# Optimization experiments

Measured on AMD Instinct MI355X. Metric: run time of the kernel, lower is better.

Reference implementation:

```python
import jax, jax.numpy as jnp
import numpy as np

P = 0.5  # dropout fraction (init kwarg p)


def setup_inputs() -> dict:
    key = jax.random.key(0)
    # positive weights (e.g. post-softmax attention), shape [B, M, N]
    w = jax.random.uniform(key, (8192, 1, 4096), dtype=jnp.float32, minval=1e-4, maxval=1.0)
    return {"w": w}


def reference(w) -> jnp.ndarray:
    # Drop the bottom int(N*P) entries along dim 2 (per row), then renormalize
    # the surviving entries with a softmax over them; dropped entries stay 0.
    B, M, N = w.shape
    k = int(N * P)  # number of smallest entries zeroed per row
    if k == 0:
        return w
    order = jnp.argsort(w, axis=2)          # ascending order indices
    ranks = jnp.argsort(order, axis=2)      # rank of each element in its row
    keep = ranks >= k                        # True for the top (N-k) entries
    neg = jnp.finfo(w.dtype).min
    logits = jnp.where(keep, w, neg)
    m = jnp.max(logits, axis=2, keepdims=True)
    e = jnp.where(keep, jnp.exp(logits - m), 0.0)
    return e / jnp.sum(e, axis=2, keepdims=True)
```

## Files before the change

kernel.cpp:

```cpp
#include <hip/hip_runtime.h>
#include <stdint.h>

constexpr int N     = 4096;
constexpr int KSEL  = 2048;
constexpr int BLOCK = 256;
constexpr int NWAVE = BLOCK / 64;
constexpr int EPL   = 64;
constexpr int NB    = 256;
constexpr int CAP   = 64;
constexpr float P1  = 0.45f;
constexpr float P2  = 0.55f;
constexpr float BSCALE = 2560.0f;

typedef float vfloat4 __attribute__((ext_vector_type(4)));

__global__ __launch_bounds__(BLOCK, 4)
void wdrop_kernel(const float* __restrict__ w, float* __restrict__ out) {
    const int t = threadIdx.x, wid = t >> 6, lane = t & 63;
    const uint64_t row = (uint64_t)blockIdx.x * NWAVE + wid;

    __shared__ alignas(16) int hist[NWAVE][NB];
    __shared__ uint32_t cb[NWAVE][CAP];
    __shared__ int      ci[NWAVE][CAP];

    uint32_t v[EPL];
    {
        const uint4* wf = (const uint4*)(w + row * N);
        uint4 u[16];
#pragma unroll
        for (int j = 0; j < 16; ++j) u[j] = wf[j * 64 + lane];
#pragma unroll
        for (int j = 0; j < 16; ++j) {
            v[j*4+0] = u[j].x; v[j*4+1] = u[j].y;
            v[j*4+2] = u[j].z; v[j*4+3] = u[j].w;
        }
    }

    ((int4*)hist[wid])[lane] = int4{0, 0, 0, 0};
    __threadfence_block();

    int clo = 0;
#pragma unroll
    for (int e = 0; e < EPL; ++e) {
        const float f = __uint_as_float(v[e]);
        clo += (f < P1);
        if (f >= P1 && f < P2)
            atomicAdd(&hist[wid][min((int)((f - P1) * BSCALE), NB - 1)], 1);
    }
#pragma unroll
    for (int off = 32; off > 0; off >>= 1) clo += __shfl_xor(clo, off, 64);
    __threadfence_block();

    const int4 hh = ((const int4*)hist[wid])[lane];
    const int a0 = hh.x, a1 = a0 + hh.y, a2 = a1 + hh.z, a3 = a2 + hh.w;
    int sc = a3;
#pragma unroll
    for (int off = 1; off < 64; off <<= 1) {
        const int u = __shfl_up(sc, off, 64);
        if (lane >= off) sc += u;
    }
    const int base = sc - a3;
    const int tot  = __shfl(sc, 63, 64);
    bool fastp = (clo < KSEL) && (clo + tot >= KSEL);
    int selb = -1, jms = 0;
    if (fastp) {
        const int jrank = KSEL - clo;
        const int inc[4] = {base + a0, base + a1, base + a2, base + a3};
        const int exc[4] = {base, base + a0, base + a1, base + a2};
#pragma unroll
        for (int i = 0; i < 4; ++i)
            if (exc[i] < jrank && jrank <= inc[i]) {
                selb = lane * 4 + i;
                jms  = jrank - exc[i] - 1;
            }
        const unsigned long long b = __ballot(selb >= 0);
        const int src = __ffsll((unsigned long long)b) - 1;
        selb = __shfl(selb, src, 64);
        jms  = __shfl(jms,  src, 64);
    }

    uint32_t thrT = 0; int thrI = 0;
    if (fastp) {
        int cn = 0;
#pragma unroll
        for (int e = 0; e < EPL; ++e) {
            const float f = __uint_as_float(v[e]);
            const bool in = (f >= P1) && (f < P2) &&
                            (min((int)((f - P1) * BSCALE), NB - 1) == selb);
            const unsigned long long m = __ballot(in);
            if (in) {
                const int slot = cn + __popcll(m & ((1ull << lane) - 1ull));
                if (slot < CAP) {
                    cb[wid][slot] = v[e];
                    ci[wid][slot] = ((e >> 2) * 64 + lane) * 4 + (e & 3);
                }
            }
            cn += __popcll(m);
        }
        if (cn > CAP) fastp = false;
        if (fastp) {
            __threadfence_block();
            bool found = false; uint32_t myT = 0; int myI = 0;
            if (lane < cn) {
                const uint32_t myb = cb[wid][lane]; const int myi = ci[wid][lane];
                int rank = 0;
                for (int q = 0; q < cn; ++q)
                    rank += (cb[wid][q] < myb) ||
                            (cb[wid][q] == myb && ci[wid][q] < myi);
                if (rank == jms) { found = true; myT = myb; myI = myi; }
            }
            const unsigned long long b = __ballot(found);
            const int src = __ffsll((unsigned long long)b) - 1;
            thrT = (uint32_t)__shfl((int)myT, src, 64);
            thrI = __shfl(myI, src, 64);
        }
    }

    if (!fastp) {
        uint32_t blo = 0u, bhi = 0x7f7fffffu;
        while (blo < bhi) {
            const uint32_t mid = blo + ((bhi - blo) >> 1);
            int c = 0;
#pragma unroll
            for (int e = 0; e < EPL; ++e) c += (v[e] <= mid);
#pragma unroll
            for (int off = 32; off > 0; off >>= 1) c += __shfl_xor(c, off, 64);
            if (c >= KSEL) bhi = mid; else blo = mid + 1;
        }
        const uint32_t T = blo;
        int c = 0;
#pragma unroll
        for (int e = 0; e < EPL; ++e) c += (v[e] < T);
#pragma unroll
        for (int off = 32; off > 0; off >>= 1) c += __shfl_xor(c, off, 64);
        const int need = KSEL - c;
        int ilo = 0, ihi = N - 1;
        while (ilo < ihi) {
            const int imid = (ilo + ihi) >> 1;
            int cc = 0;
#pragma unroll
            for (int e = 0; e < EPL; ++e) {
                const int idx = ((e >> 2) * 64 + lane) * 4 + (e & 3);
                cc += (v[e] == T && idx <= imid);
            }
#pragma unroll
            for (int off = 32; off > 0; off >>= 1) cc += __shfl_xor(cc, off, 64);
            if (cc >= need) ihi = imid; else ilo = imid + 1;
        }
        thrT = T; thrI = ilo;
    }

    float acc = 0.0f;
#pragma unroll
    for (int e = 0; e < EPL; ++e) {
        const int idx = ((e >> 2) * 64 + lane) * 4 + (e & 3);
        const bool keep = (v[e] > thrT) || (v[e] == thrT && idx > thrI);
        const float ev = keep ? __expf(__uint_as_float(v[e])) : 0.0f;
        v[e] = __float_as_uint(ev);
        acc += ev;
    }
#pragma unroll
    for (int off = 32; off > 0; off >>= 1) acc += __shfl_xor(acc, off, 64);
    const float inv = 1.0f / acc;

    vfloat4* of = (vfloat4*)(out + row * N);
#pragma unroll
    for (int j = 0; j < 16; ++j) {
        vfloat4 o;
        o.x = __uint_as_float(v[j*4+0]) * inv;
        o.y = __uint_as_float(v[j*4+1]) * inv;
        o.z = __uint_as_float(v[j*4+2]) * inv;
        o.w = __uint_as_float(v[j*4+3]) * inv;
        __builtin_nontemporal_store(o, &of[j * 64 + lane]);
    }
}

extern "C" void kernel_launch(void* const* d_in, const int* in_sizes, int n_in,
                              void* d_out, int out_size, void* d_ws, size_t ws_size,
                              hipStream_t stream) {
    const float* w = (const float*)d_in[0];
    float* out = (float*)d_out;
    const int rows = in_sizes[0] / N;
    wdrop_kernel<<<rows / NWAVE, BLOCK, 0, stream>>>(w, out);
}
```

Baseline: 241.1 us.

## Process each row with a full block and re-read input instead of holding it in registers

Switches from one wave per row with 64 values held in registers to one 256-thread block per row with 16 values per thread. Candidate-band values go into a shared pool, and per-bucket exp sums are accumulated so the normalizer comes from the histogram plus a small candidate set. The output pass re-reads the input from global memory or cache rather than keeping it in registers. This is meant to cut register pressure and raise occupancy, at the cost of a second global read, shared-memory atomics (including float atomics), and block-wide synchronization.

```diff
diff --git a/kernel.cpp b/kernel.cpp
--- a/kernel.cpp
+++ b/kernel.cpp
@@ -4,174 +4,275 @@
 constexpr int N     = 4096;
 constexpr int KSEL  = 2048;
 constexpr int BLOCK = 256;
-constexpr int NWAVE = BLOCK / 64;
-constexpr int EPL   = 64;
+constexpr int NW    = BLOCK / 64;
+constexpr int VPT   = 4;
 constexpr int NB    = 256;
-constexpr int CAP   = 64;
+constexpr int POOL  = 768;
+constexpr int CAND  = 64;
 constexpr float P1  = 0.45f;
 constexpr float P2  = 0.55f;
 constexpr float BSCALE = 2560.0f;
 
 typedef float vfloat4 __attribute__((ext_vector_type(4)));
 
-__global__ __launch_bounds__(BLOCK, 4)
+__global__ __launch_bounds__(BLOCK, 8)
 void wdrop_kernel(const float* __restrict__ w, float* __restrict__ out) {
     const int t = threadIdx.x, wid = t >> 6, lane = t & 63;
-    const uint64_t row = (uint64_t)blockIdx.x * NWAVE + wid;
-
-    __shared__ alignas(16) int hist[NWAVE][NB];
-    __shared__ uint32_t cb[NWAVE][CAP];
-    __shared__ int      ci[NWAVE][CAP];
-
-    uint32_t v[EPL];
+    const uint64_t row = blockIdx.x;
+    const float* rp = w + row * N;
+
+    __shared__ alignas(16) int   hist[NB];
+    __shared__ alignas(16) float hsum[NB];
+    __shared__ uint2    pool[POOL];
+    __shared__ int      pcnt;
+    __shared__ int      wclo[NW];
+    __shared__ float    whigh[NW];
+    __shared__ uint32_t candB[CAND];
+    __shared__ int      candI[CAND];
+    __shared__ uint32_t bT, bI;
+    __shared__ float    bInv;
+    __shared__ int      bFlag;
+
+    hist[t] = 0;
+    hsum[t] = 0.0f;
+    if (t == 0) pcnt = 0;
+    __syncthreads();
+
+    int clo = 0;
+    float sumHigh = 0.0f;
     {
-        const uint4* wf = (const uint4*)(w + row * N);
-        uint4 u[16];
-#pragma unroll
-        for (int j = 0; j < 16; ++j) u[j] = wf[j * 64 + lane];
-#pragma unroll
-        for (int j = 0; j < 16; ++j) {
-            v[j*4+0] = u[j].x; v[j*4+1] = u[j].y;
-            v[j*4+2] = u[j].z; v[j*4+3] = u[j].w;
-        }
-    }
-
-    ((int4*)hist[wid])[lane] = int4{0, 0, 0, 0};
-    __threadfence_block();
-
-    int clo = 0;
-#pragma unroll
-    for (int e = 0; e < EPL; ++e) {
-        const float f = __uint_as_float(v[e]);
-        clo += (f < P1);
-        if (f >= P1 && f < P2)
-            atomicAdd(&hist[wid][min((int)((f - P1) * BSCALE), NB - 1)], 1);
-    }
-#pragma unroll
-    for (int off = 32; off > 0; off >>= 1) clo += __shfl_xor(clo, off, 64);
-    __threadfence_block();
-
-    const int4 hh = ((const int4*)hist[wid])[lane];
-    const int a0 = hh.x, a1 = a0 + hh.y, a2 = a1 + hh.z, a3 = a2 + hh.w;
-    int sc = a3;
-#pragma unroll
-    for (int off = 1; off < 64; off <<= 1) {
-        const int u = __shfl_up(sc, off, 64);
-        if (lane >= off) sc += u;
-    }
-    const int base = sc - a3;
-    const int tot  = __shfl(sc, 63, 64);
-    bool fastp = (clo < KSEL) && (clo + tot >= KSEL);
-    int selb = -1, jms = 0;
-    if (fastp) {
-        const int jrank = KSEL - clo;
-        const int inc[4] = {base + a0, base + a1, base + a2, base + a3};
-        const int exc[4] = {base, base + a0, base + a1, base + a2};
-#pragma unroll
-        for (int i = 0; i < 4; ++i)
-            if (exc[i] < jrank && jrank <= inc[i]) {
-                selb = lane * 4 + i;
-                jms  = jrank - exc[i] - 1;
-            }
-        const unsigned long long b = __ballot(selb >= 0);
-        const int src = __ffsll((unsigned long long)b) - 1;
-        selb = __shfl(selb, src, 64);
-        jms  = __shfl(jms,  src, 64);
-    }
-
-    uint32_t thrT = 0; int thrI = 0;
-    if (fastp) {
+        const uint4* wf = (const uint4*)rp;
+#pragma unroll
+        for (int j = 0; j < VPT; ++j) {
+            const uint4 u = wf[j * BLOCK + t];
+            const uint32_t bits[4] = {u.x, u.y, u.z, u.w};
+#pragma unroll
+            for (int c = 0; c < 4; ++c) {
+                const uint32_t b = bits[c];
+                const float f = __uint_as_float(b);
+                const bool lo = (f < P1), hi = (f >= P2);
+                clo += lo;
+                if (hi) sumHigh += __expf(f);
+                const bool in = !lo && !hi;
+                const unsigned long long m = __ballot(in);
+                if (m) {
+                    if (in) {
+                        const int bk = min((int)((f - P1) * BSCALE), NB - 1);
+                        atomicAdd(&hist[bk], 1);
+                        atomicAdd(&hsum[bk], __expf(f));
+                    }
+                    const int leader = __ffsll(m) - 1;
+                    const int cnt = __popcll(m);
+                    int base = 0;
+                    if (lane == leader) base = atomicAdd(&pcnt, cnt);
+                    base = __shfl(base, leader, 64);
+                    if (in) {
+                        const int slot =
+                            base + __popcll(m & ((1ull << lane) - 1ull));
+                        if (slot < POOL) {
+                            const int idx = (j * BLOCK + t) * 4 + c;
+                            pool[slot] = make_uint2(b, (uint32_t)idx);
+                        }
+                    }
+                }
+            }
+        }
+    }
+#pragma unroll
+    for (int off = 32; off > 0; off >>= 1) {
+        clo += __shfl_xor(clo, off, 64);
+        sumHigh += __shfl_xor(sumHigh, off, 64);
+    }
+    if (lane == 0) { wclo[wid] = clo; whigh[wid] = sumHigh; }
+    __syncthreads();
+
+    if (wid == 0) {
+        const int   cloB = wclo[0] + wclo[1] + wclo[2] + wclo[3];
+        const float sumH = whigh[0] + whigh[1] + whigh[2] + whigh[3];
+        const int4   hh = ((const int4*)hist)[lane];
+        const float4 hs = ((const float4*)hsum)[lane];
+        const int a0 = hh.x, a1 = a0 + hh.y, a2 = a1 + hh.z, a3 = a2 + hh.w;
+        const float f0 = hs.x, f1 = f0 + hs.y, f2 = f1 + hs.z, f3 = f2 + hs.w;
+        int sc = a3; float fc = f3;
+#pragma unroll
+        for (int off = 1; off < 64; off <<= 1) {
+            const int   ui = __shfl_up(sc, off, 64);
+            const float uf = __shfl_up(fc, off, 64);
+            if (lane >= off) { sc += ui; fc += uf; }
+        }
+        const int   tot  = __shfl(sc, 63, 64);
+        const float tot2 = __shfl(fc, 63, 64);
+        const int   ibase = sc - a3;
+        const float fbase = fc - f3;
+
+        bool ok = (cloB < KSEL) && (cloB + tot >= KSEL);
+        int selb = -1, jms = 0; float sumAbove = 0.0f;
+        if (ok) {
+            const int jrank = KSEL - cloB;
+            const int   inc[4] = {ibase + a0, ibase + a1, ibase + a2, ibase + a3};
+            const int   exc[4] = {ibase, ibase + a0, ibase + a1, ibase + a2};
+            const float fin[4] = {fbase + f0, fbase + f1, fbase + f2, fbase + f3};
+#pragma unroll
+            for (int i = 0; i < 4; ++i)
+                if (exc[i] < jrank && jrank <= inc[i]) {
+                    selb = lane * 4 + i;
+                    jms  = jrank - exc[i] - 1;
+                    sumAbove = tot2 - fin[i];
+                }
+            const unsigned long long bb = __ballot(selb >= 0);
+            const int src = __ffsll(bb) - 1;
+            selb = __shfl(selb, src, 64);
+            jms  = __shfl(jms,  src, 64);
+            sumAbove = __shfl(sumAbove, src, 64);
+        }
+        const int pn = pcnt;
+        if (pn > POOL) ok = false;
+
         int cn = 0;
-#pragma unroll
-        for (int e = 0; e < EPL; ++e) {
-            const float f = __uint_as_float(v[e]);
-            const bool in = (f >= P1) && (f < P2) &&
-                            (min((int)((f - P1) * BSCALE), NB - 1) == selb);
-            const unsigned long long m = __ballot(in);
-            if (in) {
-                const int slot = cn + __popcll(m & ((1ull << lane) - 1ull));
-                if (slot < CAP) {
-                    cb[wid][slot] = v[e];
-                    ci[wid][slot] = ((e >> 2) * 64 + lane) * 4 + (e & 3);
-                }
-            }
-            cn += __popcll(m);
-        }
-        if (cn > CAP) fastp = false;
-        if (fastp) {
+        if (ok) {
+            for (int k = 0; k < pn; k += 64) {
+                const int id = k + lane;
+                const bool val = id < pn;
+                uint32_t pb = 0, pi = 0;
+                if (val) { const uint2 pe = pool[id]; pb = pe.x; pi = pe.y; }
+                bool in = false;
+                if (val) {
+                    const float pf = __uint_as_float(pb);
+                    in = (min((int)((pf - P1) * BSCALE), NB - 1) == selb);
+                }
+                const unsigned long long m = __ballot(in);
+                if (in) {
+                    const int slot = cn + __popcll(m & ((1ull << lane) - 1ull));
+                    if (slot < CAND) { candB[slot] = pb; candI[slot] = (int)pi; }
+                }
+                cn += __popcll(m);
+            }
+            if (cn > CAND) ok = false;
+        }
+        if (ok) {
             __threadfence_block();
-            bool found = false; uint32_t myT = 0; int myI = 0;
+            bool found = false; uint32_t mT = 0; int mI = 0;
             if (lane < cn) {
-                const uint32_t myb = cb[wid][lane]; const int myi = ci[wid][lane];
+                const uint32_t myb = candB[lane]; const int myi = candI[lane];
                 int rank = 0;
                 for (int q = 0; q < cn; ++q)
-                    rank += (cb[wid][q] < myb) ||
-                            (cb[wid][q] == myb && ci[wid][q] < myi);
-                if (rank == jms) { found = true; myT = myb; myI = myi; }
-            }
-            const unsigned long long b = __ballot(found);
-            const int src = __ffsll((unsigned long long)b) - 1;
-            thrT = (uint32_t)__shfl((int)myT, src, 64);
-            thrI = __shfl(myI, src, 64);
-        }
-    }
-
-    if (!fastp) {
+                    rank += (candB[q] < myb) ||
+                            (candB[q] == myb && candI[q] < myi);
+                if (rank == jms) { found = true; mT = myb; mI = myi; }
+            }
+            const unsigned long long bb = __ballot(found);
+            const int src = __ffsll(bb) - 1;
+            const uint32_t T = (uint32_t)__shfl((int)mT, src, 64);
+            const int      ti = __shfl(mI, src, 64);
+            float sb = 0.0f;
+            if (lane < cn) {
+                const uint32_t cbv = candB[lane]; const int civ = candI[lane];
+                if (cbv > T || (cbv == T && civ > ti))
+                    sb = __expf(__uint_as_float(cbv));
+            }
+#pragma unroll
+            for (int off = 32; off > 0; off >>= 1) sb += __shfl_xor(sb, off, 64);
+            if (lane == 0) {
+                bT = T; bI = (uint32_t)ti;
+                bInv = 1.0f / (sumH + sumAbove + sb);
+            }
+        }
+        if (lane == 0) bFlag = ok ? 0 : 1;
+    }
+    __syncthreads();
+
+    if (bFlag) {
+        const uint4* wf = (const uint4*)rp;
         uint32_t blo = 0u, bhi = 0x7f7fffffu;
         while (blo < bhi) {
             const uint32_t mid = blo + ((bhi - blo) >> 1);
             int c = 0;
 #pragma unroll
-            for (int e = 0; e < EPL; ++e) c += (v[e] <= mid);
+            for (int j = 0; j < VPT; ++j) {
+                const uint4 u = wf[j * BLOCK + t];
+                c += (u.x <= mid) + (u.y <= mid) + (u.z <= mid) + (u.w <= mid);
+            }
 #pragma unroll
             for (int off = 32; off > 0; off >>= 1) c += __shfl_xor(c, off, 64);
-            if (c >= KSEL) bhi = mid; else blo = mid + 1;
+            if (lane == 0) wclo[wid] = c;
+            __syncthreads();
+            const int tot = wclo[0] + wclo[1] + wclo[2] + wclo[3];
+            __syncthreads();
+            if (tot >= KSEL) bhi = mid; else blo = mid + 1;
         }
         const uint32_t T = blo;
         int c = 0;
 #pragma unroll
-        for (int e = 0; e < EPL; ++e) c += (v[e] < T);
+        for (int j = 0; j < VPT; ++j) {
+            const uint4 u = wf[j * BLOCK + t];
+            c += (u.x < T) + (u.y < T) + (u.z < T) + (u.w < T);
+        }
 #pragma unroll
         for (int off = 32; off > 0; off >>= 1) c += __shfl_xor(c, off, 64);
-        const int need = KSEL - c;
+        if (lane == 0) wclo[wid] = c;
+        __syncthreads();
+        const int clt = wclo[0] + wclo[1] + wclo[2] + wclo[3];
+        __syncthreads();
+        const int need = KSEL - clt;
         int ilo = 0, ihi = N - 1;
         while (ilo < ihi) {
             const int imid = (ilo + ihi) >> 1;
             int cc = 0;
 #pragma unroll
-            for (int e = 0; e < EPL; ++e) {
-                const int idx = ((e >> 2) * 64 + lane) * 4 + (e & 3);
-                cc += (v[e] == T && idx <= imid);
+            for (int j = 0; j < VPT; ++j) {
+                const uint4 u = wf[j * BLOCK + t];
+                const int i0 = (j * BLOCK + t) * 4;
+                cc += (u.x == T && i0 + 0 <= imid) + (u.y == T && i0 + 1 <= imid) +
+                      (u.z == T && i0 + 2 <= imid) + (u.w == T && i0 + 3 <= imid);
             }
 #pragma unroll
             for (int off = 32; off > 0; off >>= 1) cc += __shfl_xor(cc, off, 64);
-            if (cc >= need) ihi = imid; else ilo = imid + 1;
-        }
-        thrT = T; thrI = ilo;
-    }
-
-    float acc = 0.0f;
-#pragma unroll
-    for (int e = 0; e < EPL; ++e) {
-        const int idx = ((e >> 2) * 64 + lane) * 4 + (e & 3);
-        const bool keep = (v[e] > thrT) || (v[e] == thrT && idx > thrI);
-        const float ev = keep ? __expf(__uint_as_float(v[e])) : 0.0f;
-        v[e] = __float_as_uint(ev);
-        acc += ev;
-    }
-#pragma unroll
-    for (int off = 32; off > 0; off >>= 1) acc += __shfl_xor(acc, off, 64);
-    const float inv = 1.0f / acc;
-
+            if (lane == 0) wclo[wid] = cc;
+            __syncthreads();
+            const int tot = wclo[0] + wclo[1] + wclo[2] + wclo[3];
+            __syncthreads();
+            if (tot >= need) ihi = imid; else ilo = imid + 1;
+        }
+        float acc = 0.0f;
+#pragma unroll
+        for (int j = 0; j < VPT; ++j) {
+            const uint4 u = wf[j * BLOCK + t];
+            const uint32_t bits[4] = {u.x, u.y, u.z, u.w};
+            const int i0 = (j * BLOCK + t) * 4;
+#pragma unroll
+            for (int cc2 = 0; cc2 < 4; ++cc2) {
+                const bool keep = (bits[cc2] > T) ||
+                                  (bits[cc2] == T && i0 + cc2 > ilo);
+                if (keep) acc += __expf(__uint_as_float(bits[cc2]));
+            }
+        }
+#pragma unroll
+        for (int off = 32; off > 0; off >>= 1) acc += __shfl_xor(acc, off, 64);
+        if (lane == 0) whigh[wid] = acc;
+        __syncthreads();
+        if (t == 0) {
+            bT = T; bI = (uint32_t)ilo;
+            bInv = 1.0f / (whigh[0] + whigh[1] + whigh[2] + whigh[3]);
+        }
+        __syncthreads();
+    }
+
+    const uint32_t T = bT; const int ti = (int)bI; const float inv = bInv;
+    const uint4* wf = (const uint4*)rp;
     vfloat4* of = (vfloat4*)(out + row * N);
 #pragma unroll
-    for (int j = 0; j < 16; ++j) {
+    for (int j = 0; j < VPT; ++j) {
+        const uint4 u = wf[j * BLOCK + t];
+        const uint32_t bits[4] = {u.x, u.y, u.z, u.w};
+        const int i0 = (j * BLOCK + t) * 4;
         vfloat4 o;
-        o.x = __uint_as_float(v[j*4+0]) * inv;
-        o.y = __uint_as_float(v[j*4+1]) * inv;
-        o.z = __uint_as_float(v[j*4+2]) * inv;
-        o.w = __uint_as_float(v[j*4+3]) * inv;
-        __builtin_nontemporal_store(o, &of[j * 64 + lane]);
+#pragma unroll
+        for (int c = 0; c < 4; ++c) {
+            const uint32_t b = bits[c];
+            const bool keep = (b > T) || (b == T && i0 + c > ti);
+            o[c] = keep ? __expf(__uint_as_float(b)) * inv : 0.0f;
+        }
+        __builtin_nontemporal_store(o, &of[j * BLOCK + t]);
     }
 }
 
@@ -181,5 +282,5 @@
     const float* w = (const float*)d_in[0];
     float* out = (float*)d_out;
     const int rows = in_sizes[0] / N;
-    wdrop_kernel<<<rows / NWAVE, BLOCK, 0, stream>>>(w, out);
+    wdrop_kernel<<<rows, BLOCK, 0, stream>>>(w, out);
 }
```

Measured after the change: 239.5 us. No clear change (-0.7%).

## Stream row from global instead of registers, pool mid-band candidates in LDS

Applied to the files above, without the earlier changes.

The kernel no longer holds all 64 values per lane in registers. It makes one streaming pass that counts low values, sums exp of high values, and pushes mid-band values with their indices into a per-wave LDS pool. Threshold selection and the partial softmax sum then work on that pool, and the output pass re-reads the row from global (expected to hit in cache) and recomputes exp. This lowers register pressure so launch bounds can rise to 6 blocks per CU, at the cost of a second global read, extra exp work, more LDS, and atomic contention on the pool counter.

```diff
diff --git a/kernel.cpp b/kernel.cpp
--- a/kernel.cpp
+++ b/kernel.cpp
@@ -4,51 +4,62 @@
 constexpr int N     = 4096;
 constexpr int KSEL  = 2048;
 constexpr int BLOCK = 256;
-constexpr int NWAVE = BLOCK / 64;
-constexpr int EPL   = 64;
+constexpr int WPB   = 4;
+constexpr int VPL   = 16;
 constexpr int NB    = 256;
-constexpr int CAP   = 64;
+constexpr int POOL  = 512;
+constexpr int CAP   = 48;
 constexpr float P1  = 0.45f;
 constexpr float P2  = 0.55f;
 constexpr float BSCALE = 2560.0f;
 
 typedef float vfloat4 __attribute__((ext_vector_type(4)));
 
-__global__ __launch_bounds__(BLOCK, 4)
+__global__ __launch_bounds__(BLOCK, 6)
 void wdrop_kernel(const float* __restrict__ w, float* __restrict__ out) {
-    const int t = threadIdx.x, wid = t >> 6, lane = t & 63;
-    const uint64_t row = (uint64_t)blockIdx.x * NWAVE + wid;
-
-    __shared__ alignas(16) int hist[NWAVE][NB];
-    __shared__ uint32_t cb[NWAVE][CAP];
-    __shared__ int      ci[NWAVE][CAP];
-
-    uint32_t v[EPL];
-    {
-        const uint4* wf = (const uint4*)(w + row * N);
-        uint4 u[16];
-#pragma unroll
-        for (int j = 0; j < 16; ++j) u[j] = wf[j * 64 + lane];
-#pragma unroll
-        for (int j = 0; j < 16; ++j) {
-            v[j*4+0] = u[j].x; v[j*4+1] = u[j].y;
-            v[j*4+2] = u[j].z; v[j*4+3] = u[j].w;
-        }
-    }
+    const int wid = threadIdx.x >> 6, lane = threadIdx.x & 63;
+    const uint64_t row = (uint64_t)blockIdx.x * WPB + wid;
+    const uint4* wf = (const uint4*)(w + row * N);
+
+    __shared__ alignas(16) int hist[WPB][NB];
+    __shared__ uint2    pool[WPB][POOL];
+    __shared__ uint32_t candB[WPB][CAP];
+    __shared__ int      candI[WPB][CAP];
+    __shared__ int      pcnt[WPB], ccnt[WPB];
 
     ((int4*)hist[wid])[lane] = int4{0, 0, 0, 0};
+    if (lane == 0) { pcnt[wid] = 0; ccnt[wid] = 0; }
     __threadfence_block();
 
     int clo = 0;
-#pragma unroll
-    for (int e = 0; e < EPL; ++e) {
-        const float f = __uint_as_float(v[e]);
-        clo += (f < P1);
-        if (f >= P1 && f < P2)
-            atomicAdd(&hist[wid][min((int)((f - P1) * BSCALE), NB - 1)], 1);
-    }
-#pragma unroll
-    for (int off = 32; off > 0; off >>= 1) clo += __shfl_xor(clo, off, 64);
+    float sumHigh = 0.0f;
+    const int lane4 = lane * 4;
+#pragma unroll
+    for (int j = 0; j < VPL; ++j) {
+        const uint4 u = wf[j * 64 + lane];
+        const uint32_t bits[4] = {u.x, u.y, u.z, u.w};
+#pragma unroll
+        for (int c = 0; c < 4; ++c) {
+            const float f = __uint_as_float(bits[c]);
+            if (f < P1) {
+                ++clo;
+            } else if (f >= P2) {
+                sumHigh += __expf(f);
+            } else {
+                const int bk = min((int)((f - P1) * BSCALE), NB - 1);
+                atomicAdd(&hist[wid][bk], 1);
+                const int slot = atomicAdd(&pcnt[wid], 1);
+                if (slot < POOL)
+                    pool[wid][slot] =
+                        make_uint2(bits[c], (uint32_t)(j * 256 + lane4 + c));
+            }
+        }
+    }
+#pragma unroll
+    for (int off = 32; off > 0; off >>= 1) {
+        clo += __shfl_xor(clo, off, 64);
+        sumHigh += __shfl_xor(sumHigh, off, 64);
+    }
     __threadfence_block();
 
     const int4 hh = ((const int4*)hist[wid])[lane];
@@ -61,9 +72,11 @@
     }
     const int base = sc - a3;
     const int tot  = __shfl(sc, 63, 64);
-    bool fastp = (clo < KSEL) && (clo + tot >= KSEL);
+    const int pn   = pcnt[wid];
+
+    bool ok = (clo < KSEL) && (clo + tot >= KSEL) && (pn <= POOL);
     int selb = -1, jms = 0;
-    if (fastp) {
+    if (ok) {
         const int jrank = KSEL - clo;
         const int inc[4] = {base + a0, base + a1, base + a2, base + a3};
         const int exc[4] = {base, base + a0, base + a1, base + a2};
@@ -73,64 +86,84 @@
                 selb = lane * 4 + i;
                 jms  = jrank - exc[i] - 1;
             }
-        const unsigned long long b = __ballot(selb >= 0);
-        const int src = __ffsll((unsigned long long)b) - 1;
+        const unsigned long long bb = __ballot(selb >= 0);
+        const int src = __ffsll(bb) - 1;
         selb = __shfl(selb, src, 64);
         jms  = __shfl(jms,  src, 64);
     }
 
-    uint32_t thrT = 0; int thrI = 0;
-    if (fastp) {
-        int cn = 0;
-#pragma unroll
-        for (int e = 0; e < EPL; ++e) {
-            const float f = __uint_as_float(v[e]);
-            const bool in = (f >= P1) && (f < P2) &&
-                            (min((int)((f - P1) * BSCALE), NB - 1) == selb);
-            const unsigned long long m = __ballot(in);
-            if (in) {
-                const int slot = cn + __popcll(m & ((1ull << lane) - 1ull));
-                if (slot < CAP) {
-                    cb[wid][slot] = v[e];
-                    ci[wid][slot] = ((e >> 2) * 64 + lane) * 4 + (e & 3);
+    uint32_t T = 0; int ti = 0; float inv = 0.0f;
+    if (ok) {
+        float sumAbove = 0.0f;
+        for (int k = 0; k < pn; k += 64) {
+            const int id = k + lane;
+            if (id < pn) {
+                const uint2 pe = pool[wid][id];
+                const float pf = __uint_as_float(pe.x);
+                const int bk = min((int)((pf - P1) * BSCALE), NB - 1);
+                if (bk > selb) {
+                    sumAbove += __expf(pf);
+                } else if (bk == selb) {
+                    const int s = atomicAdd(&ccnt[wid], 1);
+                    if (s < CAP) { candB[wid][s] = pe.x; candI[wid][s] = (int)pe.y; }
                 }
             }
-            cn += __popcll(m);
-        }
-        if (cn > CAP) fastp = false;
-        if (fastp) {
-            __threadfence_block();
-            bool found = false; uint32_t myT = 0; int myI = 0;
+        }
+#pragma unroll
+        for (int off = 32; off > 0; off >>= 1)
+            sumAbove += __shfl_xor(sumAbove, off, 64);
+        __threadfence_block();
+        const int cn = ccnt[wid];
+        if (cn > CAP) ok = false;
+        if (ok) {
+            bool found = false; uint32_t mT = 0; int mI = 0;
             if (lane < cn) {
-                const uint32_t myb = cb[wid][lane]; const int myi = ci[wid][lane];
+                const uint32_t myb = candB[wid][lane];
+                const int      myi = candI[wid][lane];
                 int rank = 0;
                 for (int q = 0; q < cn; ++q)
-                    rank += (cb[wid][q] < myb) ||
-                            (cb[wid][q] == myb && ci[wid][q] < myi);
-                if (rank == jms) { found = true; myT = myb; myI = myi; }
-            }
-            const unsigned long long b = __ballot(found);
-            const int src = __ffsll((unsigned long long)b) - 1;
-            thrT = (uint32_t)__shfl((int)myT, src, 64);
-            thrI = __shfl(myI, src, 64);
-        }
-    }
-
-    if (!fastp) {
+                    rank += (candB[wid][q] < myb) ||
+                            (candB[wid][q] == myb && candI[wid][q] < myi);
+                if (rank == jms) { found = true; mT = myb; mI = myi; }
+            }
+            const unsigned long long bb = __ballot(found);
+            const int src = __ffsll(bb) - 1;
+            T  = (uint32_t)__shfl((int)mT, src, 64);
+            ti = __shfl(mI, src, 64);
+            float sb = 0.0f;
+            if (lane < cn) {
+                const uint32_t cbv = candB[wid][lane];
+                const int      civ = candI[wid][lane];
+                if (cbv > T || (cbv == T && civ > ti))
+                    sb = __expf(__uint_as_float(cbv));
+            }
+#pragma unroll
+            for (int off = 32; off > 0; off >>= 1) sb += __shfl_xor(sb, off, 64);
+            inv = 1.0f / (sumHigh + sumAbove + sb);
+        }
+    }
+
+    if (!ok) {
         uint32_t blo = 0u, bhi = 0x7f7fffffu;
         while (blo < bhi) {
             const uint32_t mid = blo + ((bhi - blo) >> 1);
             int c = 0;
 #pragma unroll
-            for (int e = 0; e < EPL; ++e) c += (v[e] <= mid);
+            for (int j = 0; j < VPL; ++j) {
+                const uint4 u = wf[j * 64 + lane];
+                c += (u.x <= mid) + (u.y <= mid) + (u.z <= mid) + (u.w <= mid);
+            }
 #pragma unroll
             for (int off = 32; off > 0; off >>= 1) c += __shfl_xor(c, off, 64);
             if (c >= KSEL) bhi = mid; else blo = mid + 1;
         }
-        const uint32_t T = blo;
+        T = blo;
         int c = 0;
 #pragma unroll
-        for (int e = 0; e < EPL; ++e) c += (v[e] < T);
+        for (int j = 0; j < VPL; ++j) {
+            const uint4 u = wf[j * 64 + lane];
+            c += (u.x < T) + (u.y < T) + (u.z < T) + (u.w < T);
+        }
 #pragma unroll
         for (int off = 32; off > 0; off >>= 1) c += __shfl_xor(c, off, 64);
         const int need = KSEL - c;
@@ -139,38 +172,47 @@
             const int imid = (ilo + ihi) >> 1;
             int cc = 0;
 #pragma unroll
-            for (int e = 0; e < EPL; ++e) {
-                const int idx = ((e >> 2) * 64 + lane) * 4 + (e & 3);
-                cc += (v[e] == T && idx <= imid);
+            for (int j = 0; j < VPL; ++j) {
+                const uint4 u = wf[j * 64 + lane];
+                const int i0 = j * 256 + lane4;
+                cc += (u.x == T && i0 + 0 <= imid) + (u.y == T && i0 + 1 <= imid) +
+                      (u.z == T && i0 + 2 <= imid) + (u.w == T && i0 + 3 <= imid);
             }
 #pragma unroll
             for (int off = 32; off > 0; off >>= 1) cc += __shfl_xor(cc, off, 64);
             if (cc >= need) ihi = imid; else ilo = imid + 1;
         }
-        thrT = T; thrI = ilo;
-    }
-
-    float acc = 0.0f;
-#pragma unroll
-    for (int e = 0; e < EPL; ++e) {
-        const int idx = ((e >> 2) * 64 + lane) * 4 + (e & 3);
-        const bool keep = (v[e] > thrT) || (v[e] == thrT && idx > thrI);
-        const float ev = keep ? __expf(__uint_as_float(v[e])) : 0.0f;
-        v[e] = __float_as_uint(ev);
-        acc += ev;
-    }
-#pragma unroll
-    for (int off = 32; off > 0; off >>= 1) acc += __shfl_xor(acc, off, 64);
-    const float inv = 1.0f / acc;
+        ti = ilo;
+        float acc = 0.0f;
+#pragma unroll
+        for (int j = 0; j < VPL; ++j) {
+            const uint4 u = wf[j * 64 + lane];
+            const uint32_t bits[4] = {u.x, u.y, u.z, u.w};
+            const int i0 = j * 256 + lane4;
+#pragma unroll
+            for (int c2 = 0; c2 < 4; ++c2) {
+                const bool keep = (bits[c2] > T) || (bits[c2] == T && i0 + c2 > ti);
+                if (keep) acc += __expf(__uint_as_float(bits[c2]));
+            }
+        }
+#pragma unroll
+        for (int off = 32; off > 0; off >>= 1) acc += __shfl_xor(acc, off, 64);
+        inv = 1.0f / acc;
+    }
 
     vfloat4* of = (vfloat4*)(out + row * N);
 #pragma unroll
-    for (int j = 0; j < 16; ++j) {
+    for (int j = 0; j < VPL; ++j) {
+        const uint4 u = wf[j * 64 + lane];
+        const uint32_t bits[4] = {u.x, u.y, u.z, u.w};
+        const int i0 = j * 256 + lane4;
         vfloat4 o;
-        o.x = __uint_as_float(v[j*4+0]) * inv;
-        o.y = __uint_as_float(v[j*4+1]) * inv;
-        o.z = __uint_as_float(v[j*4+2]) * inv;
-        o.w = __uint_as_float(v[j*4+3]) * inv;
+#pragma unroll
+        for (int c = 0; c < 4; ++c) {
+            const uint32_t b = bits[c];
+            const bool keep = (b > T) || (b == T && i0 + c > ti);
+            o[c] = keep ? __expf(__uint_as_float(b)) * inv : 0.0f;
+        }
         __builtin_nontemporal_store(o, &of[j * 64 + lane]);
     }
 }
@@ -181,5 +223,5 @@
     const float* w = (const float*)d_in[0];
     float* out = (float*)d_out;
     const int rows = in_sizes[0] / N;
-    wdrop_kernel<<<rows / NWAVE, BLOCK, 0, stream>>>(w, out);
+    wdrop_kernel<<<rows / WPB, BLOCK, 0, stream>>>(w, out);
 }
```

New measurement: 299.0 us. +24.0%, slower.
